# Kernel tuning notes

Hardware: AMD Instinct MI355X
Metric: run time of the kernel (lower is better)

The kernel has to match this reference:

```python
import jax, jax.numpy as jnp
import numpy as np

B, T, D = 2, 2048, 2048
H, HD = 16, 128
HHD = HD // 2
SCALE = 1.0 / np.sqrt(HHD).astype(np.float32)


def setup_inputs() -> dict:
    key = jax.random.key(0)
    ks = jax.random.split(key, 6)
    s = 1.0 / np.sqrt(D).astype(np.float32)
    return {
        "x": jax.random.normal(ks[0], (B, T, D), jnp.float32),
        "Wq": jax.random.normal(ks[1], (D, H * HD), jnp.float32) * s,
        "Wk": jax.random.normal(ks[2], (D, H * HD), jnp.float32) * s,
        "Wv": jax.random.normal(ks[3], (D, H * HD), jnp.float32) * s,
        "Wo": jax.random.normal(ks[4], (H * HD, D), jnp.float32) * s,
        "lambda_init": jnp.full((H,), -0.2, jnp.float32),
    }


def reference(x, Wq, Wk, Wv, Wo, lambda_init):
    b, t, d = x.shape
    # projections -> (B, H, T, HD)
    q = (x @ Wq).reshape(b, t, H, HD).transpose(0, 2, 1, 3)
    k = (x @ Wk).reshape(b, t, H, HD).transpose(0, 2, 1, 3)
    v = (x @ Wv).reshape(b, t, H, HD).transpose(0, 2, 1, 3)
    q1, q2 = q[..., :HHD], q[..., HHD:]
    k1, k2 = k[..., :HHD], k[..., HHD:]
    scores1 = jnp.einsum('bhtc,bhsc->bhts', q1, k1) * SCALE
    scores2 = jnp.einsum('bhtc,bhsc->bhts', q2, k2) * SCALE
    causal = jnp.tril(jnp.ones((t, t), bool))  # (T, T)
    neg_inf = jnp.float32(-jnp.inf)
    scores1 = jnp.where(causal[None, None], scores1, neg_inf)
    scores2 = jnp.where(causal[None, None], scores2, neg_inf)
    attn1 = jax.nn.softmax(scores1, axis=-1)
    attn2 = jax.nn.softmax(scores2, axis=-1)
    lam = jax.nn.sigmoid(lambda_init)[None, :, None, None]
    diff_attn = attn1 - lam * attn2
    out = jnp.einsum('bhts,bhsd->bhtd', diff_attn, v)
    out = out.transpose(0, 2, 1, 3).reshape(b, t, H * HD)
    return out @ Wo
```

## Files before the change

### kernel.cpp

```cpp
#include <hip/hip_runtime.h>
#include <cstdint>
#include <cstddef>


typedef unsigned short u16;
typedef __bf16 bf16x8 __attribute__((ext_vector_type(8)));
typedef float f32x4 __attribute__((ext_vector_type(4)));

#define LOG2E 1.44269504088896340736f
#define KS 0.18033688011112042f
#define CB 11.541560327111707f

__device__ __forceinline__ u16 f2bu(float f) {
  unsigned int x = __float_as_uint(f);
  x += 0x7fffu + ((x >> 16) & 1u);
  return (u16)(x >> 16);
}

__device__ __forceinline__ void stage16(const void* g, void* lds_uniform, int lane) {
#if defined(__has_builtin) && __has_builtin(__builtin_amdgcn_global_load_lds)
  (void)lane;
  __builtin_amdgcn_global_load_lds(
      (__attribute__((address_space(1))) void*)(g),
      (__attribute__((address_space(3))) void*)(lds_uniform), 16, 0, 0);
#else
  *(uint4*)((char*)lds_uniform + lane * 16) = *(const uint4*)g;
#endif
}

__global__ void f32_to_bf16_k(const float* __restrict__ in, u16* __restrict__ out, int n4) {
  int i = blockIdx.x * blockDim.x + threadIdx.x;
  if (i < n4) {
    float4 v = ((const float4*)in)[i];
    ushort4 u;
    u.x = f2bu(v.x); u.y = f2bu(v.y); u.z = f2bu(v.z); u.w = f2bu(v.w);
    ((ushort4*)out)[i] = u;
  }
}

__global__ void transpose_f32_bf16(const float* __restrict__ in, u16* __restrict__ out,
                                   int R, int C) {
  __shared__ u16 tile[32][33];
  const int tx = threadIdx.x & 31, ty = threadIdx.x >> 5;
  const int c0 = blockIdx.x * 32, r0 = blockIdx.y * 32;
#pragma unroll
  for (int i = 0; i < 32; i += 8)
    tile[ty + i][tx] = f2bu(in[(size_t)(r0 + ty + i) * C + c0 + tx]);
  __syncthreads();
#pragma unroll
  for (int i = 0; i < 32; i += 8)
    out[(size_t)(c0 + ty + i) * R + r0 + tx] = tile[tx][ty + i];
}

template <int MODE>
__global__ void gemm_bt(const u16* __restrict__ A, const u16* __restrict__ BT,
                        void* __restrict__ C, u16* __restrict__ C2,
                        int Mdim, int Ndim, int Kdim) {
  __shared__ __align__(16) u16 As[128 * 32];
  __shared__ __align__(16) u16 Bs[128 * 32];
  const int tid = threadIdx.x;
  const int lane = tid & 63;
  const int w = tid >> 6;
  const int wm = w & 1, wn = w >> 1;
  const int li = lane & 15, lh = lane >> 4;
  const int m0 = blockIdx.x * 128;
  const int n0 = blockIdx.y * 128;

  const f32x4 fzero = {0.f, 0.f, 0.f, 0.f};
  f32x4 acc[4][4];
#pragma unroll
  for (int i = 0; i < 4; ++i)
#pragma unroll
    for (int jj = 0; jj < 4; ++jj) acc[i][jj] = fzero;

  for (int k0 = 0; k0 < Kdim; k0 += 32) {
#pragma unroll
    for (int i = 0; i < 2; ++i) {
      const int c = i * 256 + w * 64 + lane;
      stage16(A + (size_t)(m0 + (c >> 2)) * Kdim + k0 + ((c & 3) << 3),
              (char*)As + (size_t)(i * 256 + w * 64) * 16, lane);
      stage16(BT + (size_t)(n0 + (c >> 2)) * Kdim + k0 + ((c & 3) << 3),
              (char*)Bs + (size_t)(i * 256 + w * 64) * 16, lane);
    }
    __syncthreads();

    bf16x8 af[4], bfr[4];
#pragma unroll
    for (int mt = 0; mt < 4; ++mt)
      af[mt] = *(const bf16x8*)&As[(wm * 64 + mt * 16 + li) * 32 + lh * 8];
#pragma unroll
    for (int nt = 0; nt < 4; ++nt)
      bfr[nt] = *(const bf16x8*)&Bs[(wn * 64 + nt * 16 + li) * 32 + lh * 8];
#pragma unroll
    for (int mt = 0; mt < 4; ++mt)
#pragma unroll
      for (int nt = 0; nt < 4; ++nt)
        acc[mt][nt] = __builtin_amdgcn_mfma_f32_16x16x32_bf16(af[mt], bfr[nt], acc[mt][nt], 0, 0, 0);
    __syncthreads();
  }

#pragma unroll
  for (int mt = 0; mt < 4; ++mt) {
#pragma unroll
    for (int nt = 0; nt < 4; ++nt) {
      const int mb = m0 + wm * 64 + mt * 16 + lh * 4;
      const int n = n0 + wn * 64 + nt * 16 + li;
      if (MODE == 0) {
        u16* o = (u16*)C;
#pragma unroll
        for (int r = 0; r < 4; ++r)
          o[(size_t)(mb + r) * Ndim + n] = f2bu(acc[mt][nt][r]);
      } else if (MODE == 1) {
        float* o = (float*)C;
#pragma unroll
        for (int r = 0; r < 4; ++r)
          o[(size_t)(mb + r) * Ndim + n] = acc[mt][nt][r];
      } else if (MODE == 2) {
        u16* o = (u16*)C;
        const int bb = mb >> 11, t = mb & 2047;
        const int hh = n >> 7, d = n & 127;
        ushort4 u;
        u.x = f2bu(acc[mt][nt][0]);
        u.y = f2bu(acc[mt][nt][1]);
        u.z = f2bu(acc[mt][nt][2]);
        u.w = f2bu(acc[mt][nt][3]);
        *(ushort4*)&o[((size_t)((bb * 16 + hh) * 128 + d) << 11) + t] = u;
      } else {
        const int proj = n >> 11;
        const int nn = n & 2047;
        if (proj < 2) {
          u16* o = (u16*)C + (size_t)proj * 4096 * 2048;
#pragma unroll
          for (int r = 0; r < 4; ++r)
            o[(size_t)(mb + r) * 2048 + nn] = f2bu(acc[mt][nt][r]);
        } else {
          const int bb = mb >> 11, t = mb & 2047;
          const int hh = nn >> 7, d = nn & 127;
          ushort4 u;
          u.x = f2bu(acc[mt][nt][0]);
          u.y = f2bu(acc[mt][nt][1]);
          u.z = f2bu(acc[mt][nt][2]);
          u.w = f2bu(acc[mt][nt][3]);
          *(ushort4*)&C2[((size_t)((bb * 16 + hh) * 128 + d) << 11) + t] = u;
        }
      }
    }
  }
}

__device__ __forceinline__ void stage_kv(const u16* __restrict__ kbase,
                                         const u16* __restrict__ vbase, int j,
                                         u16* ksBuf, u16* vsBuf, int w, int lane) {
  const int kst_r = lane >> 4, kst_c = lane & 15;
  const int vst_r = lane >> 3, vst_c = lane & 7;
#pragma unroll
  for (int i = 0; i < 4; ++i) {
    const int t = w * 4 + i;
    const int srow = t * 4 + kst_r;
    const int scb = kst_c ^ (srow & 7);
    stage16(kbase + (size_t)(j * 64 + srow) * 2048 + scb * 8,
            (char*)ksBuf + t * 1024, lane);
    const int drow = t * 8 + vst_r;
    const int dcb = vst_c ^ (drow & 7);
    stage16(vbase + (size_t)drow * 2048 + j * 64 + dcb * 8,
            (char*)vsBuf + t * 1024, lane);
  }
}

__global__ __launch_bounds__(256, 2)
void diff_attn(const u16* __restrict__ Q, const u16* __restrict__ K,
               const u16* __restrict__ VT, const float* __restrict__ lamin,
               u16* __restrict__ AO) {
  __shared__ __align__(16) u16 Ks[2][64 * 128];
  __shared__ __align__(16) u16 Vs[2][128 * 64];
  __shared__ __align__(16) u16 Ps1[64 * 64];
  __shared__ __align__(16) u16 Ps2[64 * 64];

  const int tid = threadIdx.x, lane = tid & 63, w = tid >> 6;
  const int li = lane & 15, lh = lane >> 4;
  const int bh = blockIdx.x & 31, pair = blockIdx.x >> 5;
  const int b = bh >> 4, h = bh & 15;

  const float lam = 1.f / (1.f + exp2f(-lamin[h] * LOG2E));
  const u16* kbase = K + ((size_t)(b * 2048)) * 2048 + h * 128;
  const u16* vbase = VT + ((size_t)(b * 16 + h) << 18);
  const f32x4 fzero = {0.f, 0.f, 0.f, 0.f};

  for (int phase = 0; phase < 2; ++phase) {
    const int it = phase ? 31 - pair : pair;
    const int t0 = it * 64;

    bf16x8 qf[4];
    {
      const u16* qp = Q + (size_t)(b * 2048 + t0 + w * 16 + li) * 2048 + h * 128 + lh * 8;
#pragma unroll
      for (int kk = 0; kk < 4; ++kk) qf[kk] = *(const bf16x8*)(qp + kk * 32);
    }

    f32x4 o1[8], o2[8];
#pragma unroll
    for (int i = 0; i < 8; ++i) { o1[i] = fzero; o2[i] = fzero; }
    float l1p[4] = {0.f, 0.f, 0.f, 0.f};
    float l2p[4] = {0.f, 0.f, 0.f, 0.f};

    if (phase) __syncthreads();
    stage_kv(kbase, vbase, 0, Ks[0], Vs[0], w, lane);

    for (int j = 0; j <= it; ++j) {
      const int cur = j & 1;
      __syncthreads();
      if (j < it)
        stage_kv(kbase, vbase, j + 1, Ks[cur ^ 1], Vs[cur ^ 1], w, lane);

      const u16* __restrict__ ks = Ks[cur];
      const u16* __restrict__ vs = Vs[cur];
      const bool diag = (j == it);

#pragma unroll
      for (int nt = 0; nt < 4; ++nt) {
        const int srow = nt * 16 + li;
        const int sw = li & 7;
        bf16x8 b0 = *(const bf16x8*)&ks[srow * 128 + ((0 + lh) ^ sw) * 8];
        bf16x8 b1 = *(const bf16x8*)&ks[srow * 128 + ((4 + lh) ^ sw) * 8];
        bf16x8 b2 = *(const bf16x8*)&ks[srow * 128 + ((8 + lh) ^ sw) * 8];
        bf16x8 b3 = *(const bf16x8*)&ks[srow * 128 + ((12 + lh) ^ sw) * 8];
        f32x4 s1 = fzero, s2 = fzero;
        s1 = __builtin_amdgcn_mfma_f32_16x16x32_bf16(qf[0], b0, s1, 0, 0, 0);
        s1 = __builtin_amdgcn_mfma_f32_16x16x32_bf16(qf[1], b1, s1, 0, 0, 0);
        s2 = __builtin_amdgcn_mfma_f32_16x16x32_bf16(qf[2], b2, s2, 0, 0, 0);
        s2 = __builtin_amdgcn_mfma_f32_16x16x32_bf16(qf[3], b3, s2, 0, 0, 0);

        const int cb = nt * 2 + (li >> 3);
        const int sg = j * 64 + nt * 16 + li;
#pragma unroll
        for (int r = 0; r < 4; ++r) {
          const int row = w * 16 + lh * 4 + r;
          float p1, p2;
          if (diag && sg > t0 + row) {
            p1 = 0.f; p2 = 0.f;
          } else {
            p1 = exp2f(fmaf(s1[r], KS, -CB));
            p2 = exp2f(fmaf(s2[r], KS, -CB));
          }
          l1p[r] += p1; l2p[r] += p2;
          const int idx = row * 64 + ((cb ^ (row & 7)) << 3) + (li & 7);
          Ps1[idx] = f2bu(p1);
          Ps2[idx] = f2bu(p2);
        }
      }

#pragma unroll
      for (int kss = 0; kss < 2; ++kss) {
        const int arow = w * 16 + li;
        const int jb = ((kss * 4 + lh) ^ (li & 7)) * 8;
        bf16x8 a1f = *(const bf16x8*)&Ps1[arow * 64 + jb];
        bf16x8 a2f = *(const bf16x8*)&Ps2[arow * 64 + jb];
#pragma unroll
        for (int nt = 0; nt < 8; ++nt) {
          const int d = nt * 16 + li;
          bf16x8 vf = *(const bf16x8*)&vs[d * 64 + ((kss * 4 + lh) ^ (li & 7)) * 8];
          o1[nt] = __builtin_amdgcn_mfma_f32_16x16x32_bf16(a1f, vf, o1[nt], 0, 0, 0);
          o2[nt] = __builtin_amdgcn_mfma_f32_16x16x32_bf16(a2f, vf, o2[nt], 0, 0, 0);
        }
      }
    }

#pragma unroll
    for (int r = 0; r < 4; ++r) {
#pragma unroll
      for (int off = 1; off < 16; off <<= 1) {
        l1p[r] += __shfl_xor(l1p[r], off);
        l2p[r] += __shfl_xor(l2p[r], off);
      }
    }

#pragma unroll
    for (int r = 0; r < 4; ++r) {
      const float inv1 = 1.f / l1p[r];
      const float inv2 = lam / l2p[r];
      u16* orow = AO + (size_t)(b * 2048 + t0 + w * 16 + lh * 4 + r) * 2048 + h * 128 + li;
#pragma unroll
      for (int nt = 0; nt < 8; ++nt)
        orow[nt * 16] = f2bu(o1[nt][r] * inv1 - o2[nt][r] * inv2);
    }
  }
}

extern "C" void kernel_launch(void* const* d_in, const int* in_sizes, int n_in,
                              void* d_out, int out_size, void* d_ws, size_t ws_size,
                              hipStream_t stream) {
  const float* x   = (const float*)d_in[0];
  const float* Wq  = (const float*)d_in[1];
  const float* Wk  = (const float*)d_in[2];
  const float* Wv  = (const float*)d_in[3];
  const float* Wo  = (const float*)d_in[4];
  const float* lam = (const float*)d_in[5];
  float* out = (float*)d_out;

  const size_t MB = 1ull << 20;
  char* ws = (char*)d_ws;
  u16* qb = (u16*)d_out;
  u16* kb = qb + (size_t)4096 * 2048;

  if (ws_size >= 56 * MB) {
    u16* xb = (u16*)(ws);
    u16* wT = (u16*)(ws + 16 * MB);
    u16* vt = (u16*)(ws + 40 * MB);
    u16* ao = xb;

    f32_to_bf16_k<<<8192, 256, 0, stream>>>(x, xb, 2097152);
    transpose_f32_bf16<<<dim3(64, 64), 256, 0, stream>>>(Wq, wT, 2048, 2048);
    transpose_f32_bf16<<<dim3(64, 64), 256, 0, stream>>>(Wk, wT + (size_t)4 * MB, 2048, 2048);
    transpose_f32_bf16<<<dim3(64, 64), 256, 0, stream>>>(Wv, wT + (size_t)8 * MB, 2048, 2048);
    gemm_bt<3><<<dim3(32, 48), 256, 0, stream>>>(xb, wT, qb, vt, 4096, 6144, 2048);

    diff_attn<<<dim3(512), 256, 0, stream>>>(qb, kb, vt, lam, ao);

    transpose_f32_bf16<<<dim3(64, 64), 256, 0, stream>>>(Wo, wT, 2048, 2048);
    gemm_bt<1><<<dim3(32, 16), 256, 0, stream>>>(ao, wT, out, nullptr, 4096, 2048, 2048);
  } else {
    u16* xb = (u16*)(ws);
    u16* wT = (u16*)(ws + 16 * MB);
    u16* vt = (u16*)(ws + 24 * MB);
    u16* ao = xb;

    f32_to_bf16_k<<<8192, 256, 0, stream>>>(x, xb, 2097152);
    transpose_f32_bf16<<<dim3(64, 64), 256, 0, stream>>>(Wq, wT, 2048, 2048);
    gemm_bt<0><<<dim3(32, 16), 256, 0, stream>>>(xb, wT, qb, nullptr, 4096, 2048, 2048);
    transpose_f32_bf16<<<dim3(64, 64), 256, 0, stream>>>(Wk, wT, 2048, 2048);
    gemm_bt<0><<<dim3(32, 16), 256, 0, stream>>>(xb, wT, kb, nullptr, 4096, 2048, 2048);
    transpose_f32_bf16<<<dim3(64, 64), 256, 0, stream>>>(Wv, wT, 2048, 2048);
    gemm_bt<2><<<dim3(32, 16), 256, 0, stream>>>(xb, wT, vt, nullptr, 4096, 2048, 2048);

    diff_attn<<<dim3(512), 256, 0, stream>>>(qb, kb, vt, lam, ao);

    transpose_f32_bf16<<<dim3(64, 64), 256, 0, stream>>>(Wo, wT, 2048, 2048);
    gemm_bt<1><<<dim3(32, 16), 256, 0, stream>>>(ao, wT, out, nullptr, 4096, 2048, 2048);
  }
}
```

Before: 408.9 us.

## Replace fused QKV GEMM with 256x256-tile, 8-wave pipelined kernel with XCD-aware tile mapping

Adds a new QKV projection GEMM that uses 256x256 output tiles with 512 threads. K-slices are staged through multi-buffered swizzled LDS (5 A slots, 4 B slots) using direct global-to-LDS loads. Each K step is split into four phases that interleave staging, barriers and MFMA with setprio, and block IDs are mapped so each XCD handles a fixed set of N tiles for L2 reuse. The aim is to raise arithmetic intensity and overlap memory with compute in the largest GEMM, at the cost of more LDS and registers per block and fewer blocks per CU.

New measurement: 410.5 us. Within noise of the previous version (+0.4%).

```diff
diff --git a/kernel.cpp b/kernel.cpp
--- a/kernel.cpp
+++ b/kernel.cpp
@@ -115,7 +115,7 @@
 #pragma unroll
         for (int r = 0; r < 4; ++r)
           o[(size_t)(mb + r) * Ndim + n] = acc[mt][nt][r];
-      } else if (MODE == 2) {
+      } else {
         u16* o = (u16*)C;
         const int bb = mb >> 11, t = mb & 2047;
         const int hh = n >> 7, d = n & 127;
@@ -125,24 +125,138 @@
         u.z = f2bu(acc[mt][nt][2]);
         u.w = f2bu(acc[mt][nt][3]);
         *(ushort4*)&o[((size_t)((bb * 16 + hh) * 128 + d) << 11) + t] = u;
+      }
+    }
+  }
+}
+
+__device__ __forceinline__ void stage_half256(const u16* __restrict__ gbase, int Kdim,
+                                              u16* lds_slot, int tid) {
+#pragma unroll
+  for (int j = 0; j < 2; ++j) {
+    const int c = j * 512 + tid;
+    const int ks = c >> 9;
+    const int o = (c & 511) << 4;
+    const int osz = o ^ (((o >> 9) & 1) << 5);
+    const int row = osz >> 6;
+    const int kel = (osz & 63) >> 1;
+    stage16(gbase + (size_t)row * Kdim + ks * 32 + kel,
+            (char*)lds_slot + ((size_t)(j * 512 + (tid & ~63)) << 4), tid & 63);
+  }
+}
+
+#define PHASE256(MH, KS, LOADB, STAGESTMT, TAILSTMT)                           \
+  {                                                                            \
+    bf16x8 af[4];                                                              \
+    _Pragma("unroll")                                                          \
+    for (int mq = 0; mq < 4; ++mq)                                             \
+      af[mq] = *(const bf16x8*)&As[sA][KS][((MH)*4 + mq) * 16 + li][lhx8];     \
+    if (LOADB) {                                                               \
+      _Pragma("unroll")                                                        \
+      for (int nt = 0; nt < 4; ++nt)                                           \
+        bfc[nt] = *(const bf16x8*)&Bs[sB][KS][brow + nt * 16 + li][lhx8];      \
+    }                                                                          \
+    STAGESTMT;                                                                 \
+    __builtin_amdgcn_s_barrier();                                              \
+    asm volatile("" ::: "memory");                                             \
+    __builtin_amdgcn_s_setprio(1);                                             \
+    _Pragma("unroll")                                                          \
+    for (int mq = 0; mq < 4; ++mq) {                                           \
+      _Pragma("unroll")                                                        \
+      for (int nt = 0; nt < 4; ++nt)                                           \
+        acc[(MH)*4 + mq][nt] = __builtin_amdgcn_mfma_f32_16x16x32_bf16(        \
+            af[mq], bfc[nt], acc[(MH)*4 + mq][nt], 0, 0, 0);                   \
+    }                                                                          \
+    __builtin_amdgcn_s_setprio(0);                                             \
+    TAILSTMT;                                                                  \
+    __builtin_amdgcn_s_barrier();                                              \
+    asm volatile("" ::: "memory");                                             \
+  }
+
+__global__ __launch_bounds__(512, 2)
+void gemm256_qkv(const u16* __restrict__ A, const u16* __restrict__ BT,
+                 u16* __restrict__ C, u16* __restrict__ C2, int Kdim) {
+  __shared__ __align__(16) u16 As[5][2][128][32];
+  __shared__ __align__(16) u16 Bs[4][2][128][32];
+
+  const int tid = threadIdx.x;
+  const int lane = tid & 63;
+  const int w = tid >> 6;
+  const int wm = w >> 2;
+  const int wn = w & 3;
+  const int li = lane & 15, lh = lane >> 4;
+  const int lhx8 = (lh ^ (((li >> 3) & 1) << 1)) * 8;
+  const int brow = (wn & 1) * 64;
+
+  const int bid = blockIdx.x;
+  const int xcd = bid & 7;
+  const int local = bid >> 3;
+  const int mtile = local / 3;
+  const int ntile = xcd * 3 + (local % 3);
+  const int m0 = mtile * 256, n0 = ntile * 256;
+
+  const int NT = Kdim >> 6;
+  const u16* Abase = A + (size_t)m0 * Kdim;
+  const u16* Bbase = BT + (size_t)n0 * Kdim;
+
+  auto stA = [&](int g) {
+    if (g < 2 * NT)
+      stage_half256(Abase + (size_t)((g & 1) * 128) * Kdim + (g >> 1) * 64, Kdim,
+                    &As[g % 5][0][0][0], tid);
+  };
+  auto stB = [&](int g) {
+    if (g < 2 * NT)
+      stage_half256(Bbase + (size_t)((g & 1) * 128) * Kdim + (g >> 1) * 64, Kdim,
+                    &Bs[g & 3][0][0][0], tid);
+  };
+
+  const f32x4 fzero = {0.f, 0.f, 0.f, 0.f};
+  f32x4 acc[8][4];
+#pragma unroll
+  for (int i = 0; i < 8; ++i)
+#pragma unroll
+    for (int jj = 0; jj < 4; ++jj) acc[i][jj] = fzero;
+
+  stA(0); stB(0); stA(1); stB(1); stA(2);
+  asm volatile("s_waitcnt vmcnt(2)" ::: "memory");
+  __builtin_amdgcn_s_barrier();
+  asm volatile("" ::: "memory");
+
+  bf16x8 bfc[4];
+  for (int kt = 0; kt < NT; ++kt) {
+    const int sA = (2 * kt + wm) % 5;
+    const int sB = (2 * kt + (wn >> 1)) & 3;
+    PHASE256(0, 0, 1, stA(2 * kt + 3), ((void)0));
+    PHASE256(1, 0, 0, stB(2 * kt + 2), ((void)0));
+    PHASE256(0, 1, 1, stB(2 * kt + 3), ((void)0));
+    PHASE256(1, 1, 0, stA(2 * kt + 4),
+             if (kt + 2 < NT) { asm volatile("s_waitcnt vmcnt(2)" ::: "memory"); }
+             else             { asm volatile("s_waitcnt vmcnt(0)" ::: "memory"); });
+  }
+
+  const int proj = n0 >> 11;
+  const int nB = (n0 & 2047) + wn * 64;
+  const int mB = m0 + wm * 128;
+#pragma unroll
+  for (int mt = 0; mt < 8; ++mt) {
+#pragma unroll
+    for (int nt = 0; nt < 4; ++nt) {
+      const int mb = mB + mt * 16 + lh * 4;
+      const int n = nB + nt * 16 + li;
+      if (proj < 2) {
+        u16* o = C + (size_t)proj * 4096 * 2048;
+#pragma unroll
+        for (int r = 0; r < 4; ++r)
+          o[(size_t)(mb + r) * 2048 + n] = f2bu(acc[mt][nt][r]);
       } else {
-        const int proj = n >> 11;
-        const int nn = n & 2047;
-        if (proj < 2) {
-          u16* o = (u16*)C + (size_t)proj * 4096 * 2048;
-#pragma unroll
-          for (int r = 0; r < 4; ++r)
-            o[(size_t)(mb + r) * 2048 + nn] = f2bu(acc[mt][nt][r]);
-        } else {
-          const int bb = mb >> 11, t = mb & 2047;
-          const int hh = nn >> 7, d = nn & 127;
-          ushort4 u;
-          u.x = f2bu(acc[mt][nt][0]);
-          u.y = f2bu(acc[mt][nt][1]);
-          u.z = f2bu(acc[mt][nt][2]);
-          u.w = f2bu(acc[mt][nt][3]);
-          *(ushort4*)&C2[((size_t)((bb * 16 + hh) * 128 + d) << 11) + t] = u;
-        }
+        const int bb = mb >> 11, t = mb & 2047;
+        const int hh = n >> 7, d = n & 127;
+        ushort4 u;
+        u.x = f2bu(acc[mt][nt][0]);
+        u.y = f2bu(acc[mt][nt][1]);
+        u.z = f2bu(acc[mt][nt][2]);
+        u.w = f2bu(acc[mt][nt][3]);
+        *(ushort4*)&C2[((size_t)((bb * 16 + hh) * 128 + d) << 11) + t] = u;
       }
     }
   }
@@ -312,7 +426,7 @@
     transpose_f32_bf16<<<dim3(64, 64), 256, 0, stream>>>(Wq, wT, 2048, 2048);
     transpose_f32_bf16<<<dim3(64, 64), 256, 0, stream>>>(Wk, wT + (size_t)4 * MB, 2048, 2048);
     transpose_f32_bf16<<<dim3(64, 64), 256, 0, stream>>>(Wv, wT + (size_t)8 * MB, 2048, 2048);
-    gemm_bt<3><<<dim3(32, 48), 256, 0, stream>>>(xb, wT, qb, vt, 4096, 6144, 2048);
+    gemm256_qkv<<<dim3(384), 512, 0, stream>>>(xb, wT, qb, vt, 2048);
 
     diff_attn<<<dim3(512), 256, 0, stream>>>(qb, kb, vt, lam, ao);
 
```
